# Kernel optimization log

Measured on AMD Instinct MI355X. Metric: run time of the kernel, lower is better.

Reference implementation:

```python
import jax, jax.numpy as jnp
import numpy as np


def setup_inputs() -> dict:
    key = jax.random.key(0)
    ks = jax.random.split(key, 8)
    B, C, H, W = 16, 512, 96, 96
    Cr = C // 8
    s = 0.02
    return {
        "x": jax.random.normal(ks[0], (B, C, H, W), jnp.float32),
        "Wq": jax.random.normal(ks[1], (Cr, C), jnp.float32) * s,
        "bq": jax.random.normal(ks[2], (Cr,), jnp.float32) * s,
        "Wk": jax.random.normal(ks[3], (Cr, C), jnp.float32) * s,
        "bk": jax.random.normal(ks[4], (Cr,), jnp.float32) * s,
        "Wv": jax.random.normal(ks[5], (C, C), jnp.float32) * s,
        "bv": jax.random.normal(ks[6], (C,), jnp.float32) * s,
        "gamma": jax.random.normal(ks[7], (1,), jnp.float32) * 0.1,
    }


def _conv1x1(x, W, b):
    # 1x1 conv == channel contraction: [B,C,H,W] x [O,C] -> [B,O,H,W]
    return jnp.einsum('bchw,oc->bohw', x, W) + b[None, :, None, None]


def reference(x, Wq, bq, Wk, bk, Wv, bv, gamma):
    B, C, H, W = x.shape
    q = _conv1x1(x, Wq, bq)   # [B,Cr,H,W]
    k = _conv1x1(x, Wk, bk)   # [B,Cr,H,W]
    v = _conv1x1(x, Wv, bv)   # [B,C,H,W]

    # energy along column (vertical): query at (i,w), keys at (j,w) -> [B,H,W,H]
    eh = jnp.einsum('bciw,bcjw->biwj', q, k)
    # energy along row (horizontal): query at (h,i), keys at (h,j) -> [B,H,W,W]
    ew = jnp.einsum('bchi,bchj->bhij', q, k)

    attn = jax.nn.softmax(jnp.concatenate([eh, ew], axis=-1), axis=-1)  # [B,H,W,H+W]
    ah = attn[..., :H]   # [B,H,W,H]
    aw = attn[..., H:]   # [B,H,W,W]

    out_h = jnp.einsum('bcjw,biwj->bciw', v, ah)  # vertical aggregation
    out_w = jnp.einsum('bchj,bhij->bchi', v, aw)  # horizontal aggregation
    out = out_h + out_w
    return gamma[0] * out + x
```

## Files before the change

kernel.cpp:

```cpp
#include <hip/hip_runtime.h>
#include <hip/hip_bf16.h>

#define DI __device__ __forceinline__

typedef short bf16x8 __attribute__((ext_vector_type(8)));
typedef float f32x4 __attribute__((ext_vector_type(4)));
typedef unsigned short u16;
typedef u16 u16x2 __attribute__((ext_vector_type(2)));
typedef u16 u16x4 __attribute__((ext_vector_type(4)));
typedef u16 u16x8 __attribute__((ext_vector_type(8)));

#define B_ 16
#define C_ 512
#define CR_ 64
#define H_ 96
#define HW_ 9216
#define K_ 512

DI float b2f(u16 u){ unsigned v = ((unsigned)u)<<16; float f; __builtin_memcpy(&f,&v,4); return f; }
DI u16 f2b(float f){ unsigned v; __builtin_memcpy(&v,&f,4); v += 0x7fff + ((v>>16)&1); return (u16)(v>>16); }

DI void gload16(const void* g, void* l){
  __builtin_amdgcn_global_load_lds((const __attribute__((address_space(1))) unsigned*)g,
                                   (__attribute__((address_space(3))) unsigned*)l, 16, 0, 0);
}

__global__ __launch_bounds__(256) void k_pack(const float* __restrict__ Wq, const float* __restrict__ bq,
    const float* __restrict__ Wk, const float* __restrict__ bk,
    const float* __restrict__ Wv, const float* __restrict__ bv,
    u16* __restrict__ Wcat, float* __restrict__ bcat){
  int gid = blockIdx.x*256 + threadIdx.x;
  int o = gid >> 9, c = gid & 511;
  float w = (o < 64) ? Wq[o*512 + c] : (o < 128) ? Wk[(o-64)*512 + c] : Wv[(o-128)*512 + c];
  Wcat[gid] = f2b(w);
  if (c == 0) bcat[o] = (o < 64) ? bq[o] : (o < 128) ? bk[o-64] : bv[o-128];
}

__global__ __launch_bounds__(256) void k_xt(const float* __restrict__ x, u16* __restrict__ xt){
  int bx = blockIdx.x;
  int pt = bx % 144; int ct = (bx/144) & 7; int b = bx / (144*8);
  __shared__ u16 T[64*72];
  const float* xb = x + (size_t)b*C_*HW_ + (size_t)(ct*64)*HW_ + pt*64;
  for (int it = threadIdx.x; it < 1024; it += 256){
    int r = it & 63, px4 = it >> 6;
    f32x4 f4 = *(const f32x4*)(xb + (size_t)r*HW_ + px4*4);
    #pragma unroll
    for (int e=0;e<4;++e) T[(px4*4 + e)*72 + r] = f2b(f4[e]);
  }
  __syncthreads();
  u16* xtb = xt + (size_t)b*HW_*K_ + (size_t)(pt*64)*K_ + ct*64;
  for (int it = threadIdx.x; it < 512; it += 256){
    int c8 = it & 7, p = it >> 3;
    u16x8 o;
    #pragma unroll
    for (int e=0;e<8;++e) o[e] = T[p*72 + c8*8 + e];
    *(u16x8*)(xtb + (size_t)p*K_ + c8*8) = o;
  }
}

__global__ __launch_bounds__(256) void k_qkv(const u16* __restrict__ Wcat, const float* __restrict__ bcat,
    const u16* __restrict__ xt, u16* __restrict__ q, u16* __restrict__ k, u16* __restrict__ v){
  int bx = blockIdx.x;
  int wg = (bx & 7)*720 + (bx >> 3);
  int nt = wg % 72; int tmp = wg / 72; int mt = tmp % 5; int b = tmp / 5;
  __shared__ u16 As[128*64];
  __shared__ u16 Bs[128*64];
  int lane = threadIdx.x & 63, wid = threadIdx.x >> 6;
  int wr = wid >> 1, wc = wid & 1;
  const u16* xb = xt + (size_t)b*HW_*K_ + (size_t)nt*128*K_;
  const u16* Ab = Wcat + (size_t)mt*128*K_;

  f32x4 acc[4][4];
  #pragma unroll
  for (int i=0;i<4;++i)
    #pragma unroll
    for (int j=0;j<4;++j) acc[i][j] = (f32x4){0.f,0.f,0.f,0.f};

  int ibase = wid*4;
  for (int kt=0; kt<8; ++kt){
    int k0 = kt*64;
    __syncthreads();
    #pragma unroll
    for (int i=0;i<4;++i){
      int byteL = ((ibase + i)<<10) + (lane<<4);
      int row = byteL >> 7;
      int slog = ((byteL >> 4) & 7) ^ (row & 7);
      size_t ge = (size_t)row*K_ + (k0 + slog*8);
      gload16(Ab + ge, (char*)As + ((ibase+i)<<10));
      gload16(xb + ge, (char*)Bs + ((ibase+i)<<10));
    }
    __syncthreads();
    bf16x8 af[4][2], bfr[4][2];
    #pragma unroll
    for (int f=0; f<4; ++f){
      #pragma unroll
      for (int kk=0; kk<2; ++kk){
        int sl = kk*4 + (lane >> 4);
        int ra = wr*64 + f*16 + (lane & 15);
        af[f][kk]  = *(const bf16x8*)((const char*)As + ra*128 + ((sl ^ (ra & 7))<<4));
        int rb = wc*64 + f*16 + (lane & 15);
        bfr[f][kk] = *(const bf16x8*)((const char*)Bs + rb*128 + ((sl ^ (rb & 7))<<4));
      }
    }
    #pragma unroll
    for (int fm=0; fm<4; ++fm)
      #pragma unroll
      for (int fn=0; fn<4; ++fn)
        #pragma unroll
        for (int kk=0; kk<2; ++kk)
          acc[fm][fn] = __builtin_amdgcn_mfma_f32_16x16x32_bf16(af[fm][kk], bfr[fn][kk], acc[fm][fn], 0, 0, 0);
  }
  int r4 = lane >> 4, cl = lane & 15;
  for (int fm=0; fm<4; ++fm){
    for (int j=0;j<4;++j){
      int o = mt*128 + wr*64 + fm*16 + r4*4 + j;
      float bias = bcat[o];
      for (int fn=0; fn<4; ++fn){
        int n = nt*128 + wc*64 + fn*16 + cl;
        u16 bv16 = f2b(acc[fm][fn][j] + bias);
        if (o < 64)       q[((size_t)b*CR_ + o)*HW_ + n] = bv16;
        else if (o < 128) k[((size_t)b*CR_ + (o-64))*HW_ + n] = bv16;
        else              v[((size_t)b*C_ + (o-128))*HW_ + n] = bv16;
      }
    }
  }
}

__global__ __launch_bounds__(256) void k_tr(const u16* __restrict__ q, const u16* __restrict__ kk,
    const u16* __restrict__ v, u16* __restrict__ qt, u16* __restrict__ kt, u16* __restrict__ vt){
  int bx = blockIdx.x;
  int ch = bx % 640; int b = bx / 640;
  const u16* src; u16* dst;
  if (ch < 64)      { src = q  + ((size_t)b*CR_ + ch)*HW_;     dst = qt + ((size_t)b*CR_ + ch)*HW_; }
  else if (ch < 128){ src = kk + ((size_t)b*CR_ + ch-64)*HW_;  dst = kt + ((size_t)b*CR_ + ch-64)*HW_; }
  else              { src = v  + ((size_t)b*C_ + ch-128)*HW_;  dst = vt + ((size_t)b*C_ + ch-128)*HW_; }
  __shared__ u16 T[96*128];
  for (int it = threadIdx.x; it < 1152; it += 256){
    int h = it / 12, c8 = it % 12;
    u16x8 v8 = *(const u16x8*)(src + h*96 + c8*8);
    int sp = (h >> 3) ^ (c8 & 7);
    #pragma unroll
    for (int e = 0; e < 8; ++e){
      int w = c8*8 + e;
      T[w*128 + sp*8 + (h & 7)] = v8[e];
    }
  }
  __syncthreads();
  for (int it = threadIdx.x; it < 1152; it += 256){
    int w = it / 12, h8 = it % 12;
    int sp = h8 ^ ((w >> 3) & 7);
    u16x8 o = *(const u16x8*)&T[w*128 + sp*8];
    *(u16x8*)(dst + (size_t)w*96 + h8*8) = o;
  }
}

__global__ __launch_bounds__(256) void k_scores(const u16* __restrict__ q, const u16* __restrict__ k,
    const u16* __restrict__ qt, const u16* __restrict__ kt, u16* __restrict__ att){
  int bx = blockIdx.x;
  int p = bx % 96; int b = (bx/96) & 15; int mode = bx / 1536;
  __shared__ float Qs[64*96];
  __shared__ float Ks[64*96];
  const u16* qsrc; const u16* ksrc;
  if (mode == 0){ qsrc = qt + (size_t)b*CR_*HW_ + p*96; ksrc = kt + (size_t)b*CR_*HW_ + p*96; }
  else          { qsrc = q  + (size_t)b*CR_*HW_ + p*96; ksrc = k  + (size_t)b*CR_*HW_ + p*96; }
  for (int u = threadIdx.x; u < 64*12; u += 256){
    int c = u / 12, ch = u % 12;
    u16x8 a = *(const u16x8*)(qsrc + (size_t)c*HW_ + ch*8);
    u16x8 d = *(const u16x8*)(ksrc + (size_t)c*HW_ + ch*8);
    #pragma unroll
    for (int e=0;e<8;++e){ Qs[c*96 + ch*8 + e] = b2f(a[e]); Ks[c*96 + ch*8 + e] = b2f(d[e]); }
  }
  __syncthreads();
  int ti = threadIdx.x >> 4, tj = threadIdx.x & 15;
  float acc[6][6];
  #pragma unroll
  for (int a2=0;a2<6;++a2)
    #pragma unroll
    for (int b2=0;b2<6;++b2) acc[a2][b2] = 0.f;
  for (int c=0;c<64;++c){
    float qv[6], kv[6];
    #pragma unroll
    for (int a2=0;a2<6;++a2){ qv[a2] = Qs[c*96 + ti + 16*a2]; kv[a2] = Ks[c*96 + tj + 16*a2]; }
    #pragma unroll
    for (int a2=0;a2<6;++a2)
      #pragma unroll
      for (int b2=0;b2<6;++b2) acc[a2][b2] += qv[a2]*kv[b2];
  }
  for (int a2=0;a2<6;++a2){
    int i = ti + 16*a2;
    for (int b2=0;b2<6;++b2){
      int j = tj + 16*b2;
      size_t idx = (mode==0) ? ((size_t)((b*96 + i)*96 + p))*192 + j
                             : ((size_t)((b*96 + p)*96 + i))*192 + 96 + j;
      att[idx] = f2b(acc[a2][b2]);
    }
  }
}

__global__ __launch_bounds__(256) void k_softmax(u16* __restrict__ att){
  int row = blockIdx.x*8 + (threadIdx.x >> 5);
  int sub = threadIdx.x & 31;
  u16* r = att + (size_t)row*192 + sub*6;
  u16x2 a = *(u16x2*)r, b = *(u16x2*)(r+2), c = *(u16x2*)(r+4);
  float v0=b2f(a[0]),v1=b2f(a[1]),v2=b2f(b[0]),v3=b2f(b[1]),v4=b2f(c[0]),v5=b2f(c[1]);
  float m = fmaxf(fmaxf(fmaxf(v0,v1),fmaxf(v2,v3)),fmaxf(v4,v5));
  #pragma unroll
  for (int off=16; off; off>>=1) m = fmaxf(m, __shfl_xor(m, off));
  float e0=__expf(v0-m),e1=__expf(v1-m),e2=__expf(v2-m),e3=__expf(v3-m),e4=__expf(v4-m),e5=__expf(v5-m);
  float s = ((e0+e1)+(e2+e3))+(e4+e5);
  #pragma unroll
  for (int off=16; off; off>>=1) s += __shfl_xor(s, off);
  float inv = 1.0f/s;
  a[0]=f2b(e0*inv); a[1]=f2b(e1*inv); b[0]=f2b(e2*inv); b[1]=f2b(e3*inv); c[0]=f2b(e4*inv); c[1]=f2b(e5*inv);
  *(u16x2*)r = a; *(u16x2*)(r+2) = b; *(u16x2*)(r+4) = c;
}

__global__ __launch_bounds__(512) void k_outh(u16* vo, const u16* __restrict__ att){
  int bx = blockIdx.x; int w = bx % 96, b = bx / 96;
  __shared__ u16 Ah[96*104];
  for (int u = threadIdx.x; u < 96*48; u += 512){
    int i = u/48, jc = u%48;
    *(u16x2*)&Ah[i*104 + jc*2] = *(const u16x2*)(att + ((size_t)((b*96 + i)*96 + w))*192 + jc*2);
  }
  __syncthreads();
  int lane = threadIdx.x & 63, wid = threadIdx.x >> 6;
  int cl = lane & 15, r4 = lane >> 4;
  f32x4 acc[4][6];
  #pragma unroll
  for (int i=0;i<4;++i)
    #pragma unroll
    for (int j=0;j<6;++j) acc[i][j] = (f32x4){0.f,0.f,0.f,0.f};
  u16* vb = vo + (size_t)b*C_*HW_ + (size_t)w*96;
  #pragma unroll
  for (int kt=0; kt<3; ++kt){
    int kof = kt*32 + r4*8;
    bf16x8 a[4], bb[6];
    #pragma unroll
    for (int fm=0; fm<4; ++fm){
      int c = wid*64 + fm*16 + cl;
      a[fm] = *(const bf16x8*)(vb + (size_t)c*HW_ + kof);
    }
    #pragma unroll
    for (int fn=0; fn<6; ++fn)
      bb[fn] = *(const bf16x8*)&Ah[(fn*16 + cl)*104 + kof];
    #pragma unroll
    for (int fm=0; fm<4; ++fm)
      #pragma unroll
      for (int fn=0; fn<6; ++fn)
        acc[fm][fn] = __builtin_amdgcn_mfma_f32_16x16x32_bf16(a[fm], bb[fn], acc[fm][fn], 0, 0, 0);
  }
  for (int fm=0; fm<4; ++fm)
    for (int fn=0; fn<6; ++fn)
      for (int j=0;j<4;++j){
        int c = wid*64 + fm*16 + r4*4 + j;
        int i = fn*16 + cl;
        vb[(size_t)c*HW_ + i] = f2b(acc[fm][fn][j]);
      }
}

__global__ __launch_bounds__(512) void k_outw(u16* vo, const u16* __restrict__ att){
  int bx = blockIdx.x; int h = bx % 96, b = bx / 96;
  __shared__ u16 Aw[96*104];
  for (int u = threadIdx.x; u < 96*48; u += 512){
    int i = u/48, jc = u%48;
    *(u16x2*)&Aw[i*104 + jc*2] = *(const u16x2*)(att + ((size_t)((b*96 + h)*96 + i))*192 + 96 + jc*2);
  }
  __syncthreads();
  int lane = threadIdx.x & 63, wid = threadIdx.x >> 6;
  int cl = lane & 15, r4 = lane >> 4;
  f32x4 acc[4][6];
  #pragma unroll
  for (int i=0;i<4;++i)
    #pragma unroll
    for (int j=0;j<6;++j) acc[i][j] = (f32x4){0.f,0.f,0.f,0.f};
  u16* vb = vo + (size_t)b*C_*HW_ + (size_t)h*96;
  #pragma unroll
  for (int kt=0; kt<3; ++kt){
    int kof = kt*32 + r4*8;
    bf16x8 a[4], bb[6];
    #pragma unroll
    for (int fm=0; fm<4; ++fm){
      int c = wid*64 + fm*16 + cl;
      a[fm] = *(const bf16x8*)(vb + (size_t)c*HW_ + kof);
    }
    #pragma unroll
    for (int fn=0; fn<6; ++fn)
      bb[fn] = *(const bf16x8*)&Aw[(fn*16 + cl)*104 + kof];
    #pragma unroll
    for (int fm=0; fm<4; ++fm)
      #pragma unroll
      for (int fn=0; fn<6; ++fn)
        acc[fm][fn] = __builtin_amdgcn_mfma_f32_16x16x32_bf16(a[fm], bb[fn], acc[fm][fn], 0, 0, 0);
  }
  for (int fm=0; fm<4; ++fm)
    for (int fn=0; fn<6; ++fn)
      for (int j=0;j<4;++j){
        int c = wid*64 + fm*16 + r4*4 + j;
        int i = fn*16 + cl;
        vb[(size_t)c*HW_ + i] = f2b(acc[fm][fn][j]);
      }
}

__global__ __launch_bounds__(256) void k_final(const u16* oh, const u16* ow,
    const float* __restrict__ x, const float* __restrict__ gp, float* __restrict__ out){
  int bx = blockIdx.x; int c = bx & 511; int b = bx >> 9;
  size_t base = ((size_t)b*C_ + c)*HW_;
  const u16* ohc = oh + base;
  const u16* owc = ow + base;
  __shared__ u16 T[96*128];
  for (int it = threadIdx.x; it < 1152; it += 256){
    int w = it / 12, c8 = it % 12;
    u16x8 v8 = *(const u16x8*)(ohc + w*96 + c8*8);
    int sp = (w >> 3) ^ (c8 & 7);
    #pragma unroll
    for (int e = 0; e < 8; ++e){
      int i = c8*8 + e;
      T[i*128 + sp*8 + (w & 7)] = v8[e];
    }
  }
  __syncthreads();
  float g = gp[0];
  for (int it = threadIdx.x; it < 2304; it += 256){
    int i = it / 24, w4 = it % 24; int w = w4*4;
    int sp = (w >> 3) ^ ((i >> 3) & 7);
    u16x4 t4 = *(const u16x4*)&T[i*128 + sp*8 + (w & 7)];
    u16x4 o4 = *(const u16x4*)(owc + i*96 + w);
    f32x4 x4 = *(const f32x4*)(x + base + i*96 + w);
    f32x4 r;
    #pragma unroll
    for (int e=0;e<4;++e) r[e] = g*(b2f(t4[e]) + b2f(o4[e])) + x4[e];
    *(f32x4*)(out + base + i*96 + w) = r;
  }
}

extern "C" void kernel_launch(void* const* d_in, const int* in_sizes, int n_in,
                              void* d_out, int out_size, void* d_ws, size_t ws_size,
                              hipStream_t stream) {
  (void)in_sizes; (void)n_in; (void)out_size; (void)ws_size;
  const float* x  = (const float*)d_in[0];
  const float* Wq = (const float*)d_in[1];
  const float* bq = (const float*)d_in[2];
  const float* Wk = (const float*)d_in[3];
  const float* bk = (const float*)d_in[4];
  const float* Wv = (const float*)d_in[5];
  const float* bv = (const float*)d_in[6];
  const float* gm = (const float*)d_in[7];
  float* out = (float*)d_out;
  char* ws = (char*)d_ws;

  u16*  Wcat = (u16*)(ws);
  float* bcat= (float*)(ws + 655360);
  u16*  q    = (u16*)(ws + 659456);
  u16*  k    = (u16*)(ws + 19533824);
  u16*  qt   = (u16*)(ws + 38408192);
  u16*  kt   = (u16*)(ws + 57282560);
  u16*  v    = (u16*)(ws + 76156928);
  u16*  att  = (u16*)(ws + 227151872);
  u16*  vt   = (u16*)(ws + 283774976);
  u16*  xt   = (u16*)d_out;

  k_pack   <<<1280, 256, 0, stream>>>(Wq,bq,Wk,bk,Wv,bv,Wcat,bcat);
  k_xt     <<<18432,256, 0, stream>>>(x, xt);
  k_qkv    <<<5760, 256, 0, stream>>>(Wcat,bcat,xt,q,k,v);
  k_tr     <<<10240,256, 0, stream>>>(q,k,v,qt,kt,vt);
  k_scores <<<3072, 256, 0, stream>>>(q,k,qt,kt,att);
  k_softmax<<<18432,256, 0, stream>>>(att);
  k_outh   <<<1536, 512, 0, stream>>>(vt,att);
  k_outw   <<<1536, 512, 0, stream>>>(v,att);
  k_final  <<<8192, 256, 0, stream>>>(vt,v,x,gm,out);
}
```

Before: 824.6 us.

## Double-buffer LDS tiles in QKV GEMM and reorder block mapping

Adds a second LDS buffer to the QKV projection GEMM so the global-to-LDS loads for the next K tile are issued before the MFMA work on the current tile, which is meant to hide load latency and drop one barrier per iteration. The workgroup index decomposition also changes so that the five M-tiles sharing one x tile are adjacent, which should improve L2 reuse of the x tile. The cost is doubled shared memory use (64KB per block), which may reduce occupancy.

```diff
diff --git a/kernel.cpp b/kernel.cpp
--- a/kernel.cpp
+++ b/kernel.cpp
@@ -62,9 +62,9 @@
     const u16* __restrict__ xt, u16* __restrict__ q, u16* __restrict__ k, u16* __restrict__ v){
   int bx = blockIdx.x;
   int wg = (bx & 7)*720 + (bx >> 3);
-  int nt = wg % 72; int tmp = wg / 72; int mt = tmp % 5; int b = tmp / 5;
-  __shared__ u16 As[128*64];
-  __shared__ u16 Bs[128*64];
+  int mt = wg % 5; int rest = wg / 5; int nt = rest % 72; int b = rest / 72;
+  __shared__ u16 As[2][128*64];
+  __shared__ u16 Bs[2][128*64];
   int lane = threadIdx.x & 63, wid = threadIdx.x >> 6;
   int wr = wid >> 1, wc = wid & 1;
   const u16* xb = xt + (size_t)b*HW_*K_ + (size_t)nt*128*K_;
@@ -77,19 +77,34 @@
     for (int j=0;j<4;++j) acc[i][j] = (f32x4){0.f,0.f,0.f,0.f};
 
   int ibase = wid*4;
+  int dOff[4], geB[4];
+  #pragma unroll
+  for (int i=0;i<4;++i){
+    dOff[i] = (ibase + i)<<10;
+    int byteL = dOff[i] + (lane<<4);
+    int row = byteL >> 7;
+    int slog = ((byteL >> 4) & 7) ^ (row & 7);
+    geB[i] = row*K_ + slog*8;
+  }
+
+  #pragma unroll
+  for (int i=0;i<4;++i){
+    gload16(Ab + geB[i], (char*)As[0] + dOff[i]);
+    gload16(xb + geB[i], (char*)Bs[0] + dOff[i]);
+  }
+  __syncthreads();
+
+  int cur = 0;
+  #pragma unroll
   for (int kt=0; kt<8; ++kt){
-    int k0 = kt*64;
-    __syncthreads();
-    #pragma unroll
-    for (int i=0;i<4;++i){
-      int byteL = ((ibase + i)<<10) + (lane<<4);
-      int row = byteL >> 7;
-      int slog = ((byteL >> 4) & 7) ^ (row & 7);
-      size_t ge = (size_t)row*K_ + (k0 + slog*8);
-      gload16(Ab + ge, (char*)As + ((ibase+i)<<10));
-      gload16(xb + ge, (char*)Bs + ((ibase+i)<<10));
-    }
-    __syncthreads();
+    if (kt < 7){
+      int k0 = (kt+1)*64;
+      #pragma unroll
+      for (int i=0;i<4;++i){
+        gload16(Ab + geB[i] + k0, (char*)As[cur^1] + dOff[i]);
+        gload16(xb + geB[i] + k0, (char*)Bs[cur^1] + dOff[i]);
+      }
+    }
     bf16x8 af[4][2], bfr[4][2];
     #pragma unroll
     for (int f=0; f<4; ++f){
@@ -97,9 +112,9 @@
       for (int kk=0; kk<2; ++kk){
         int sl = kk*4 + (lane >> 4);
         int ra = wr*64 + f*16 + (lane & 15);
-        af[f][kk]  = *(const bf16x8*)((const char*)As + ra*128 + ((sl ^ (ra & 7))<<4));
+        af[f][kk]  = *(const bf16x8*)((const char*)As[cur] + ra*128 + ((sl ^ (ra & 7))<<4));
         int rb = wc*64 + f*16 + (lane & 15);
-        bfr[f][kk] = *(const bf16x8*)((const char*)Bs + rb*128 + ((sl ^ (rb & 7))<<4));
+        bfr[f][kk] = *(const bf16x8*)((const char*)Bs[cur] + rb*128 + ((sl ^ (rb & 7))<<4));
       }
     }
     #pragma unroll
@@ -109,7 +124,10 @@
         #pragma unroll
         for (int kk=0; kk<2; ++kk)
           acc[fm][fn] = __builtin_amdgcn_mfma_f32_16x16x32_bf16(af[fm][kk], bfr[fn][kk], acc[fm][fn], 0, 0, 0);
-  }
+    __syncthreads();
+    cur ^= 1;
+  }
+
   int r4 = lane >> 4, cl = lane & 15;
   for (int fm=0; fm<4; ++fm){
     for (int j=0;j<4;++j){
```

Measured after the change: 884.8 us. +7.3%, slower.

## Stage QKV GEMM output through LDS for vectorized stores; reorder tiles and transpose reads

Applied to the files above, without the earlier changes.

The QKV projection epilogue now writes bias-added bf16 results into shared memory and then emits 16-byte vectorized global stores, replacing scattered 2-byte stores. The block-to-tile mapping now puts the M-tile index innermost, so the blocks sharing one xt tile run close together and can reuse it from L2. The x-transpose kernel now reads along pixels (coalesced) and uses a padded LDS stride of 80. The aim is less store and read inefficiency, at the cost of an extra LDS round trip and barriers in the epilogue.

```diff
diff --git a/kernel.cpp b/kernel.cpp
--- a/kernel.cpp
+++ b/kernel.cpp
@@ -39,13 +39,13 @@
 __global__ __launch_bounds__(256) void k_xt(const float* __restrict__ x, u16* __restrict__ xt){
   int bx = blockIdx.x;
   int pt = bx % 144; int ct = (bx/144) & 7; int b = bx / (144*8);
-  __shared__ u16 T[64*72];
+  __shared__ u16 T[64*80];
   const float* xb = x + (size_t)b*C_*HW_ + (size_t)(ct*64)*HW_ + pt*64;
   for (int it = threadIdx.x; it < 1024; it += 256){
-    int r = it & 63, px4 = it >> 6;
+    int px4 = it & 15, r = it >> 4;
     f32x4 f4 = *(const f32x4*)(xb + (size_t)r*HW_ + px4*4);
     #pragma unroll
-    for (int e=0;e<4;++e) T[(px4*4 + e)*72 + r] = f2b(f4[e]);
+    for (int e=0;e<4;++e) T[(px4*4 + e)*80 + r] = f2b(f4[e]);
   }
   __syncthreads();
   u16* xtb = xt + (size_t)b*HW_*K_ + (size_t)(pt*64)*K_ + ct*64;
@@ -53,7 +53,7 @@
     int c8 = it & 7, p = it >> 3;
     u16x8 o;
     #pragma unroll
-    for (int e=0;e<8;++e) o[e] = T[p*72 + c8*8 + e];
+    for (int e=0;e<8;++e) o[e] = T[p*80 + c8*8 + e];
     *(u16x8*)(xtb + (size_t)p*K_ + c8*8) = o;
   }
 }
@@ -62,9 +62,9 @@
     const u16* __restrict__ xt, u16* __restrict__ q, u16* __restrict__ k, u16* __restrict__ v){
   int bx = blockIdx.x;
   int wg = (bx & 7)*720 + (bx >> 3);
-  int nt = wg % 72; int tmp = wg / 72; int mt = tmp % 5; int b = tmp / 5;
-  __shared__ u16 As[128*64];
-  __shared__ u16 Bs[128*64];
+  int mt = wg % 5; int rest = wg / 5; int nt = rest % 72; int b = rest / 72;
+  __shared__ u16 S[2][128*64];
+  u16* As = S[0]; u16* Bs = S[1];
   int lane = threadIdx.x & 63, wid = threadIdx.x >> 6;
   int wr = wid >> 1, wc = wid & 1;
   const u16* xb = xt + (size_t)b*HW_*K_ + (size_t)nt*128*K_;
@@ -110,19 +110,35 @@
         for (int kk=0; kk<2; ++kk)
           acc[fm][fn] = __builtin_amdgcn_mfma_f32_16x16x32_bf16(af[fm][kk], bfr[fn][kk], acc[fm][fn], 0, 0, 0);
   }
+
+  __syncthreads();
+  u16* Cs = S[0];
   int r4 = lane >> 4, cl = lane & 15;
-  for (int fm=0; fm<4; ++fm){
-    for (int j=0;j<4;++j){
-      int o = mt*128 + wr*64 + fm*16 + r4*4 + j;
-      float bias = bcat[o];
+  #pragma unroll
+  for (int fm=0; fm<4; ++fm)
+    #pragma unroll
+    for (int j=0; j<4; ++j){
+      int row = wr*64 + fm*16 + r4*4 + j;
+      float bias = bcat[mt*128 + row];
+      #pragma unroll
       for (int fn=0; fn<4; ++fn){
-        int n = nt*128 + wc*64 + fn*16 + cl;
-        u16 bv16 = f2b(acc[fm][fn][j] + bias);
-        if (o < 64)       q[((size_t)b*CR_ + o)*HW_ + n] = bv16;
-        else if (o < 128) k[((size_t)b*CR_ + (o-64))*HW_ + n] = bv16;
-        else              v[((size_t)b*C_ + (o-128))*HW_ + n] = bv16;
+        int col = wc*64 + fn*16 + cl;
+        Cs[row*128 + col] = f2b(acc[fm][fn][j] + bias);
       }
     }
+  __syncthreads();
+  #pragma unroll
+  for (int i=0; i<8; ++i){
+    int chunk = i*256 + threadIdx.x;
+    int row = chunk >> 4, c8 = chunk & 15;
+    u16x8 val = *(const u16x8*)&Cs[row*128 + c8*8];
+    int o = mt*128 + row;
+    int n = nt*128 + c8*8;
+    u16* dst;
+    if (o < 64)       dst = q + ((size_t)b*CR_ + o)*HW_ + n;
+    else if (o < 128) dst = k + ((size_t)b*CR_ + (o-64))*HW_ + n;
+    else              dst = v + ((size_t)b*C_ + (o-128))*HW_ + n;
+    *(u16x8*)dst = val;
   }
 }
 
```

Measured after the change: 774.6 us. -6.1%, faster.
